# Optimization experiments

Hardware: AMD Instinct MI355X
Metric: run time of the kernel (lower is better)

The kernel has to match this reference:

```python
import jax, jax.numpy as jnp
import numpy as np

N = 8192
D = 768
TEMPERATURE = 0.1
EPS_NORM = 1e-8   # torch CosineSimilarity eps
EPS_LOG = 1e-6


def setup_inputs() -> dict:
    key = jax.random.key(0)
    k1, k2, k3 = jax.random.split(key, 3)
    features = jax.random.normal(k1, (N, D), dtype=jnp.float32)
    positive_mask = jax.random.randint(k2, (N, N), 0, 2).astype(jnp.float32)
    negative_mask = jax.random.randint(k3, (N, N), 0, 2).astype(jnp.float32)
    return {"features": features, "positive_mask": positive_mask, "negative_mask": negative_mask}


def reference(features, positive_mask, negative_mask):
    n = features.shape[0]
    # cosine similarity: normalize then GEMM (same math as broadcasted CosineSimilarity)
    norms = jnp.linalg.norm(features, axis=1, keepdims=True)
    fn = features / jnp.maximum(norms, EPS_NORM)
    sim = jnp.exp(jnp.matmul(fn, fn.T) / TEMPERATURE)  # [N, N]
    # zero out self-contrast on the diagonal of both masks
    not_eye = 1.0 - jnp.eye(n, dtype=features.dtype)
    pm = positive_mask * not_eye
    nm = negative_mask * not_eye
    pos_sums = pm.sum(axis=1)
    pos_sums = jnp.where(pos_sums == 0, 1.0, pos_sums)
    neg = jnp.sum(sim * nm, axis=1, keepdims=True)  # [N, 1]
    log_prob = -jnp.log(sim / neg + EPS_LOG)        # [N, N]
    per_row = jnp.sum(log_prob * pm, axis=1) / pos_sums
    return jnp.mean(per_row)
```

## Files before the change

kernel.cpp:

```cpp
#include <hip/hip_runtime.h>
#include <hip/hip_bf16.h>

#define NROWS 8192
#define DDIM 768

typedef short short8 __attribute__((ext_vector_type(8)));
typedef float floatx4 __attribute__((ext_vector_type(4)));
typedef unsigned long long u64;
typedef unsigned int u32;
typedef u32 u32x4 __attribute__((ext_vector_type(4)));

__global__ __launch_bounds__(256) void normalize_k(const float* __restrict__ f,
                                                   __hip_bfloat16* __restrict__ fn) {
    const int row = blockIdx.x;
    const int t = threadIdx.x;
    const float* fr = f + (size_t)row * DDIM;
    float v0 = fr[t];
    float v1 = fr[t + 256];
    float v2 = fr[t + 512];
    float ss = v0 * v0 + v1 * v1 + v2 * v2;
#pragma unroll
    for (int m = 32; m; m >>= 1) ss += __shfl_xor(ss, m, 64);
    __shared__ float wsum[4];
    if ((t & 63) == 0) wsum[t >> 6] = ss;
    __syncthreads();
    float tot = wsum[0] + wsum[1] + wsum[2] + wsum[3];
    float inv = 1.0f / fmaxf(sqrtf(tot), 1e-8f);
    __hip_bfloat16* o = fn + (size_t)row * DDIM;
    o[t]       = __float2bfloat16(v0 * inv);
    o[t + 256] = __float2bfloat16(v1 * inv);
    o[t + 512] = __float2bfloat16(v2 * inv);
}

__global__ __launch_bounds__(256) void pack_k(const float* __restrict__ pm,
                                              const float* __restrict__ nm,
                                              u32* __restrict__ pmw,
                                              u32* __restrict__ nmw,
                                              float* __restrict__ pG) {
    const int lane = threadIdx.x & 63;
    const int wv = threadIdx.x >> 6;
    const int row = blockIdx.x * 4 + wv;
    const float4* pr = (const float4*)(pm + (size_t)row * NROWS);
    const float4* nr = (const float4*)(nm + (size_t)row * NROWS);
    const int dg = row >> 8;
    const u64 dclear = ~(1ull << ((row & 255) >> 2));
    int pc = 0;
    for (int g = 0; g < 32; ++g) {
        float4 pv = pr[(size_t)g * 64 + lane];
        float4 nv = nr[(size_t)g * 64 + lane];
        u64 pb0 = __ballot(pv.x != 0.f), pb1 = __ballot(pv.y != 0.f);
        u64 pb2 = __ballot(pv.z != 0.f), pb3 = __ballot(pv.w != 0.f);
        u64 nb0 = __ballot(nv.x != 0.f), nb1 = __ballot(nv.y != 0.f);
        u64 nb2 = __ballot(nv.z != 0.f), nb3 = __ballot(nv.w != 0.f);
        if (g == dg) {
            const int dk = row & 3;
            if (dk == 0) { pb0 &= dclear; nb0 &= dclear; }
            else if (dk == 1) { pb1 &= dclear; nb1 &= dclear; }
            else if (dk == 2) { pb2 &= dclear; nb2 &= dclear; }
            else { pb3 &= dclear; nb3 &= dclear; }
        }
        pc += __popcll(pb0) + __popcll(pb1) + __popcll(pb2) + __popcll(pb3);
        const size_t wi = ((size_t)row * 32 + g) * 8;
        if (lane == 0) {
            *(u32x4*)(pmw + wi)     = (u32x4){(u32)pb0, (u32)pb1, (u32)pb2, (u32)pb3};
            *(u32x4*)(pmw + wi + 4) = (u32x4){(u32)(pb0 >> 32), (u32)(pb1 >> 32),
                                              (u32)(pb2 >> 32), (u32)(pb3 >> 32)};
        } else if (lane == 1) {
            *(u32x4*)(nmw + wi)     = (u32x4){(u32)nb0, (u32)nb1, (u32)nb2, (u32)nb3};
            *(u32x4*)(nmw + wi + 4) = (u32x4){(u32)(nb0 >> 32), (u32)(nb1 >> 32),
                                              (u32)(nb2 >> 32), (u32)(nb3 >> 32)};
        }
    }
    if (lane == 0) pG[row] = (float)pc;
}

__global__ __launch_bounds__(256, 4) void ntxent_main(
        const __hip_bfloat16* __restrict__ fn,
        const u32* __restrict__ pmw, const u32* __restrict__ nmw,
        float* __restrict__ negG, float* __restrict__ sG) {
    __shared__ __hip_bfloat16 Is[128 * 32];
    __shared__ __hip_bfloat16 Js[128 * 32];

    const int t = threadIdx.x;
    const int lane = t & 63;
    const int wv = t >> 6;
    const int wm = wv & 1;
    const int wn = wv >> 1;
    const int q  = lane >> 4;
    const int cl = lane & 15;
    const int rowBase = blockIdx.y * 128;
    const int colBase = blockIdx.x * 128;

    const int rdSw = ((q ^ ((cl >> 1) & 3)) << 4);

    floatx4 acc[4][4];
#pragma unroll
    for (int mf = 0; mf < 4; ++mf)
#pragma unroll
        for (int nf = 0; nf < 4; ++nf)
            acc[mf][nf] = (floatx4){0.f, 0.f, 0.f, 0.f};

    for (int k0 = 0; k0 < DDIM; k0 += 32) {
        __syncthreads();
#pragma unroll
        for (int it = 0; it < 2; ++it) {
            const int s = it * 256 + t;
            const int r = s >> 2;
            const int cg = (s & 3) ^ ((r >> 1) & 3);
            const __hip_bfloat16* ga = fn + (size_t)(rowBase + r) * DDIM + k0 + cg * 8;
            const __hip_bfloat16* gb = fn + (size_t)(colBase + r) * DDIM + k0 + cg * 8;
            __builtin_amdgcn_global_load_lds(
                (const __attribute__((address_space(1))) void*)ga,
                (__attribute__((address_space(3))) void*)((char*)Is + s * 16), 16, 0, 0);
            __builtin_amdgcn_global_load_lds(
                (const __attribute__((address_space(1))) void*)gb,
                (__attribute__((address_space(3))) void*)((char*)Js + s * 16), 16, 0, 0);
        }
        __syncthreads();

        short8 jf[4], if_[4];
#pragma unroll
        for (int mf = 0; mf < 4; ++mf) {
            const int r = wm * 64 + mf * 16 + cl;
            jf[mf] = *(const short8*)((const char*)Js + r * 64 + rdSw);
        }
#pragma unroll
        for (int nf = 0; nf < 4; ++nf) {
            const int r = wn * 64 + nf * 16 + cl;
            if_[nf] = *(const short8*)((const char*)Is + r * 64 + rdSw);
        }
#pragma unroll
        for (int mf = 0; mf < 4; ++mf)
#pragma unroll
            for (int nf = 0; nf < 4; ++nf)
                acc[mf][nf] = __builtin_amdgcn_mfma_f32_16x16x32_bf16(
                    jf[mf], if_[nf], acc[mf][nf], 0, 0, 0);
    }

    const int col64 = colBase + wm * 64;
    const int g = col64 >> 8;
    const int a = (col64 >> 6) & 3;
    const int hi = a >> 1;
    const int shb = (a & 1) * 16 + q;
#pragma unroll
    for (int nf = 0; nf < 4; ++nf) {
        const int grow = rowBase + wn * 64 + nf * 16 + cl;
        const size_t mb = ((size_t)grow * 32 + g) * 8 + hi * 4;
        u32x4 pu = *(const u32x4*)(pmw + mb);
        u32x4 nu = *(const u32x4*)(nmw + mb);
        float aN = 0.f, aS = 0.f;
#pragma unroll
        for (int mf = 0; mf < 4; ++mf) {
            const int sh = shb + mf * 4;
#pragma unroll
            for (int reg = 0; reg < 4; ++reg) {
                float v = acc[mf][nf][reg];
                float e = __builtin_amdgcn_exp2f(v * 14.4269504089f);
                float pb = (float)((pu[reg] >> sh) & 1u);
                float nb = (float)((nu[reg] >> sh) & 1u);
                aN = fmaf(nb, e, aN);
                aS = fmaf(pb, v, aS);
            }
        }
        aN += __shfl_xor(aN, 16, 64);  aN += __shfl_xor(aN, 32, 64);
        aS += __shfl_xor(aS, 16, 64);  aS += __shfl_xor(aS, 32, 64);
        if (q == 0) {
            atomicAdd(&negG[grow], aN);
            atomicAdd(&sG[grow],   aS);
        }
    }
}

__global__ __launch_bounds__(1024) void final_k(const float* __restrict__ negG,
        const float* __restrict__ sG, const float* __restrict__ pG,
        float* __restrict__ out) {
    const int t = threadIdx.x;
    float sum = 0.f;
    for (int i = t; i < NROWS; i += 1024) {
        float P = pG[i];
        if (P > 0.f) {
            sum += (P * logf(negG[i]) - 10.0f * sG[i]) / P;
        }
    }
#pragma unroll
    for (int m = 32; m; m >>= 1) sum += __shfl_xor(sum, m, 64);
    __shared__ float wsum[16];
    if ((t & 63) == 0) wsum[t >> 6] = sum;
    __syncthreads();
    if (t < 16) {
        float v = wsum[t];
#pragma unroll
        for (int m = 8; m; m >>= 1) v += __shfl_xor(v, m, 16);
        if (t == 0) out[0] = v / (float)NROWS;
    }
}

extern "C" void kernel_launch(void* const* d_in, const int* in_sizes, int n_in,
                              void* d_out, int out_size, void* d_ws, size_t ws_size,
                              hipStream_t stream) {
    const float* feat  = (const float*)d_in[0];
    const float* pmask = (const float*)d_in[1];
    const float* nmask = (const float*)d_in[2];
    float* out = (float*)d_out;

    char* ws = (char*)d_ws;
    __hip_bfloat16* fn = (__hip_bfloat16*)ws;
    u32* pmw = (u32*)(ws + 12582912);
    u32* nmw = (u32*)(ws + 12582912 + 8388608);
    float* negG = (float*)(ws + 12582912 + 2 * 8388608);
    float* sG = negG + NROWS;
    float* pG = sG + NROWS;

    hipMemsetAsync(negG, 0, 2 * NROWS * sizeof(float), stream);

    normalize_k<<<NROWS, 256, 0, stream>>>(feat, fn);
    pack_k<<<NROWS / 4, 256, 0, stream>>>(pmask, nmask, pmw, nmw, pG);

    dim3 grid(64, 64);
    ntxent_main<<<grid, 256, 0, stream>>>(fn, pmw, nmw, negG, sG);

    final_k<<<1, 1024, 0, stream>>>(negG, sG, pG, out);
}
```

Before: 676.9 us.

## Fuse mask reading into GEMM epilogue and drop the bit-packing kernel

Removes the separate pack kernel that turned the float masks into bitmasks and counted positives per row. The GEMM epilogue now loads the fp32 mask values directly, clears the diagonal inline, and accumulates the positive count through a third atomic. This avoids a full extra pass and the intermediate bitmask writes and reads, and lets mask traffic overlap with other blocks' matrix work. In exchange, each tile's epilogue issues strided 16-byte loads of the large float masks and one more atomic per row.

```diff
diff --git a/kernel.cpp b/kernel.cpp
--- a/kernel.cpp
+++ b/kernel.cpp
@@ -6,9 +6,6 @@
 
 typedef short short8 __attribute__((ext_vector_type(8)));
 typedef float floatx4 __attribute__((ext_vector_type(4)));
-typedef unsigned long long u64;
-typedef unsigned int u32;
-typedef u32 u32x4 __attribute__((ext_vector_type(4)));
 
 __global__ __launch_bounds__(256) void normalize_k(const float* __restrict__ f,
                                                    __hip_bfloat16* __restrict__ fn) {
@@ -32,52 +29,11 @@
     o[t + 512] = __float2bfloat16(v2 * inv);
 }
 
-__global__ __launch_bounds__(256) void pack_k(const float* __restrict__ pm,
-                                              const float* __restrict__ nm,
-                                              u32* __restrict__ pmw,
-                                              u32* __restrict__ nmw,
-                                              float* __restrict__ pG) {
-    const int lane = threadIdx.x & 63;
-    const int wv = threadIdx.x >> 6;
-    const int row = blockIdx.x * 4 + wv;
-    const float4* pr = (const float4*)(pm + (size_t)row * NROWS);
-    const float4* nr = (const float4*)(nm + (size_t)row * NROWS);
-    const int dg = row >> 8;
-    const u64 dclear = ~(1ull << ((row & 255) >> 2));
-    int pc = 0;
-    for (int g = 0; g < 32; ++g) {
-        float4 pv = pr[(size_t)g * 64 + lane];
-        float4 nv = nr[(size_t)g * 64 + lane];
-        u64 pb0 = __ballot(pv.x != 0.f), pb1 = __ballot(pv.y != 0.f);
-        u64 pb2 = __ballot(pv.z != 0.f), pb3 = __ballot(pv.w != 0.f);
-        u64 nb0 = __ballot(nv.x != 0.f), nb1 = __ballot(nv.y != 0.f);
-        u64 nb2 = __ballot(nv.z != 0.f), nb3 = __ballot(nv.w != 0.f);
-        if (g == dg) {
-            const int dk = row & 3;
-            if (dk == 0) { pb0 &= dclear; nb0 &= dclear; }
-            else if (dk == 1) { pb1 &= dclear; nb1 &= dclear; }
-            else if (dk == 2) { pb2 &= dclear; nb2 &= dclear; }
-            else { pb3 &= dclear; nb3 &= dclear; }
-        }
-        pc += __popcll(pb0) + __popcll(pb1) + __popcll(pb2) + __popcll(pb3);
-        const size_t wi = ((size_t)row * 32 + g) * 8;
-        if (lane == 0) {
-            *(u32x4*)(pmw + wi)     = (u32x4){(u32)pb0, (u32)pb1, (u32)pb2, (u32)pb3};
-            *(u32x4*)(pmw + wi + 4) = (u32x4){(u32)(pb0 >> 32), (u32)(pb1 >> 32),
-                                              (u32)(pb2 >> 32), (u32)(pb3 >> 32)};
-        } else if (lane == 1) {
-            *(u32x4*)(nmw + wi)     = (u32x4){(u32)nb0, (u32)nb1, (u32)nb2, (u32)nb3};
-            *(u32x4*)(nmw + wi + 4) = (u32x4){(u32)(nb0 >> 32), (u32)(nb1 >> 32),
-                                              (u32)(nb2 >> 32), (u32)(nb3 >> 32)};
-        }
-    }
-    if (lane == 0) pG[row] = (float)pc;
-}
-
 __global__ __launch_bounds__(256, 4) void ntxent_main(
         const __hip_bfloat16* __restrict__ fn,
-        const u32* __restrict__ pmw, const u32* __restrict__ nmw,
-        float* __restrict__ negG, float* __restrict__ sG) {
+        const float* __restrict__ pmask, const float* __restrict__ nmask,
+        float* __restrict__ negG, float* __restrict__ sG,
+        float* __restrict__ pG) {
     __shared__ __hip_bfloat16 Is[128 * 32];
     __shared__ __hip_bfloat16 Js[128 * 32];
 
@@ -138,35 +94,41 @@
     }
 
     const int col64 = colBase + wm * 64;
-    const int g = col64 >> 8;
-    const int a = (col64 >> 6) & 3;
-    const int hi = a >> 1;
-    const int shb = (a & 1) * 16 + q;
+    const int jb0 = col64 + q * 4;
 #pragma unroll
     for (int nf = 0; nf < 4; ++nf) {
         const int grow = rowBase + wn * 64 + nf * 16 + cl;
-        const size_t mb = ((size_t)grow * 32 + g) * 8 + hi * 4;
-        u32x4 pu = *(const u32x4*)(pmw + mb);
-        u32x4 nu = *(const u32x4*)(nmw + mb);
-        float aN = 0.f, aS = 0.f;
+        const float* prow = pmask + (size_t)grow * NROWS;
+        const float* nrow = nmask + (size_t)grow * NROWS;
+        float4 pm4[4], nm4[4];
 #pragma unroll
         for (int mf = 0; mf < 4; ++mf) {
-            const int sh = shb + mf * 4;
+            pm4[mf] = *(const float4*)(prow + jb0 + mf * 16);
+            nm4[mf] = *(const float4*)(nrow + jb0 + mf * 16);
+        }
+        float aN = 0.f, aS = 0.f, aP = 0.f;
+#pragma unroll
+        for (int mf = 0; mf < 4; ++mf) {
+            const int jbase = jb0 + mf * 16;
 #pragma unroll
             for (int reg = 0; reg < 4; ++reg) {
+                float pmv = ((const float*)&pm4[mf])[reg];
+                float nmv = ((const float*)&nm4[mf])[reg];
+                if (grow == jbase + reg) { pmv = 0.f; nmv = 0.f; }
                 float v = acc[mf][nf][reg];
                 float e = __builtin_amdgcn_exp2f(v * 14.4269504089f);
-                float pb = (float)((pu[reg] >> sh) & 1u);
-                float nb = (float)((nu[reg] >> sh) & 1u);
-                aN = fmaf(nb, e, aN);
-                aS = fmaf(pb, v, aS);
+                aN = fmaf(nmv, e, aN);
+                aS = fmaf(pmv, v, aS);
+                aP += pmv;
             }
         }
         aN += __shfl_xor(aN, 16, 64);  aN += __shfl_xor(aN, 32, 64);
         aS += __shfl_xor(aS, 16, 64);  aS += __shfl_xor(aS, 32, 64);
+        aP += __shfl_xor(aP, 16, 64);  aP += __shfl_xor(aP, 32, 64);
         if (q == 0) {
             atomicAdd(&negG[grow], aN);
             atomicAdd(&sG[grow],   aS);
+            atomicAdd(&pG[grow],   aP);
         }
     }
 }
@@ -205,19 +167,16 @@
 
     char* ws = (char*)d_ws;
     __hip_bfloat16* fn = (__hip_bfloat16*)ws;
-    u32* pmw = (u32*)(ws + 12582912);
-    u32* nmw = (u32*)(ws + 12582912 + 8388608);
-    float* negG = (float*)(ws + 12582912 + 2 * 8388608);
+    float* negG = (float*)(ws + 12582912);
     float* sG = negG + NROWS;
     float* pG = sG + NROWS;
 
-    hipMemsetAsync(negG, 0, 2 * NROWS * sizeof(float), stream);
+    hipMemsetAsync(negG, 0, 3 * NROWS * sizeof(float), stream);
 
     normalize_k<<<NROWS, 256, 0, stream>>>(feat, fn);
-    pack_k<<<NROWS / 4, 256, 0, stream>>>(pmask, nmask, pmw, nmw, pG);
 
     dim3 grid(64, 64);
-    ntxent_main<<<grid, 256, 0, stream>>>(fn, pmw, nmw, negG, sG);
+    ntxent_main<<<grid, 256, 0, stream>>>(fn, pmask, nmask, negG, sG, pG);
 
     final_k<<<1, 1024, 0, stream>>>(negG, sG, pG, out);
 }
```

Measured after the change: 605.9 us. -10.5%, faster.
